# Kernel optimization log

Measured on AMD Instinct MI355X. Metric: run time of the kernel, lower is better.

The kernel has to match this reference:

```python
import jax, jax.numpy as jnp
import numpy as np

N = 100000      # nodes
E = 640000      # edges
V_IN = 128
U_IN = 64
HID = 128
B = 128         # graphs


def setup_inputs() -> dict:
    key = jax.random.key(0)
    ks = jax.random.split(key, 9)
    x = jax.random.normal(ks[0], (N, V_IN), dtype=jnp.float32)
    edge_index = jax.random.randint(ks[1], (2, E), 0, N, dtype=jnp.int64)
    edge_attr = jax.random.normal(ks[2], (E, HID), dtype=jnp.float32)
    u = jax.random.normal(ks[3], (B, U_IN), dtype=jnp.float32)
    batch = jnp.sort(jax.random.randint(ks[4], (N,), 0, B, dtype=jnp.int64))
    fan_in1 = V_IN + HID + U_IN
    W1 = jax.random.normal(ks[5], (fan_in1, HID), dtype=jnp.float32) / np.sqrt(fan_in1)
    b1 = jnp.zeros((HID,), dtype=jnp.float32)
    W2 = jax.random.normal(ks[6], (HID, HID), dtype=jnp.float32) / np.sqrt(HID)
    b2 = jnp.zeros((HID,), dtype=jnp.float32)
    return {"x": x, "edge_index": edge_index, "edge_attr": edge_attr, "u": u,
            "batch": batch, "W1": W1, "b1": b1, "W2": W2, "b2": b2}


def reference(x, edge_index, edge_attr, u, batch, W1, b1, W2, b2):
    col = edge_index[1]
    # scatter_add edge_attr into destination-node slots: [N, HID]
    agg = jax.ops.segment_sum(edge_attr, col, num_segments=x.shape[0])
    # concat [x, agg, u[batch]] -> [N, V_IN + HID + U_IN]
    h = jnp.concatenate([x, agg, u[batch]], axis=1)
    h = jax.nn.relu(h @ W1 + b1)
    return h @ W2 + b2
```

## Files before the change

kernel.cpp:

```cpp
#include <hip/hip_runtime.h>
#include <hip/hip_bf16.h>

#define V_IN 128
#define U_IN 64
#define HID 128
#define K1  (V_IN + HID + U_IN)

typedef __attribute__((ext_vector_type(8))) short bf16x8;
typedef __attribute__((ext_vector_type(4))) float f32x4;

static __device__ __forceinline__ unsigned short f2bf(float f) {
    __hip_bfloat16 h = __float2bfloat16(f);
    union { __hip_bfloat16 h; unsigned short u; } v; v.h = h;
    return v.u;
}
static __device__ __forceinline__ unsigned int f2bf2(float lo, float hi) {
    __hip_bfloat162 h2 = __float22bfloat162_rn(make_float2(lo, hi));
    union { __hip_bfloat162 h; unsigned int u; } v; v.h = h2;
    return v.u;
}

__global__ __launch_bounds__(256) void zero_prep(
    const float* __restrict__ W1, const float* __restrict__ W2,
    unsigned short* __restrict__ Wt1, unsigned short* __restrict__ Wt2,
    int* __restrict__ deg, int N)
{
    int id = blockIdx.x * 256 + threadIdx.x;
    if (id < N) deg[id] = 0;
    if (id < HID * K1) {
        int c = id / K1, k = id - c * K1;
        Wt1[id] = f2bf(W1[(size_t)k * HID + c]);
    }
    if (id < HID * HID) {
        int c = id >> 7, k = id & 127;
        Wt2[id] = f2bf(W2[(size_t)k * HID + c]);
    }
}


__global__ __launch_bounds__(256) void hist_kernel(
    const int* __restrict__ col, int* __restrict__ deg, int E)
{
    int e = blockIdx.x * 256 + threadIdx.x;
    if (e < E) atomicAdd(&deg[col[e]], 1);
}

__global__ __launch_bounds__(256) void scan_partial(
    const int* __restrict__ deg, int* __restrict__ blockSums, int N)
{
    __shared__ int sdata[256];
    int base = blockIdx.x * 1024;
    int tid  = threadIdx.x;
    int s = 0;
    #pragma unroll
    for (int j = 0; j < 4; ++j) {
        int i = base + tid * 4 + j;
        if (i < N) s += deg[i];
    }
    sdata[tid] = s;
    __syncthreads();
    for (int off = 128; off > 0; off >>= 1) {
        if (tid < off) sdata[tid] += sdata[tid + off];
        __syncthreads();
    }
    if (tid == 0) blockSums[blockIdx.x] = sdata[0];
}

__global__ __launch_bounds__(256) void scan_final(
    const int* __restrict__ deg, const int* __restrict__ blockSums,
    int* __restrict__ offsets, int* __restrict__ cur, int N, int E)
{
    __shared__ int sdata[256];
    __shared__ int rdata[256];
    int tid = threadIdx.x;

    int part = 0;
    for (int i = tid; i < (int)blockIdx.x; i += 256) part += blockSums[i];
    rdata[tid] = part;
    __syncthreads();
    for (int off = 128; off > 0; off >>= 1) {
        if (tid < off) rdata[tid] += rdata[tid + off];
        __syncthreads();
    }
    const int blockPrefix = rdata[0];

    int base = blockIdx.x * 1024;
    int loc[4];
    int s = 0;
    #pragma unroll
    for (int j = 0; j < 4; ++j) {
        int i = base + tid * 4 + j;
        loc[j] = (i < N) ? deg[i] : 0;
        s += loc[j];
    }
    int mine = s;
    sdata[tid] = s;
    __syncthreads();
    for (int off = 1; off < 256; off <<= 1) {
        int t = (tid >= off) ? sdata[tid - off] : 0;
        __syncthreads();
        sdata[tid] += t;
        __syncthreads();
    }
    int prefix = blockPrefix + sdata[tid] - mine;
    #pragma unroll
    for (int j = 0; j < 4; ++j) {
        int i = base + tid * 4 + j;
        if (i < N) { offsets[i] = prefix; cur[i] = prefix; prefix += loc[j]; }
    }
    if (blockIdx.x == 0 && tid == 0) offsets[N] = E;
}

__global__ __launch_bounds__(256) void fill_kernel(
    const int* __restrict__ col, int* __restrict__ cur,
    int* __restrict__ eidx, int E)
{
    int e = blockIdx.x * 256 + threadIdx.x;
    if (e < E) {
        int p = atomicAdd(&cur[col[e]], 1);
        eidx[p] = e;
    }
}

#define ROWS 32
#define LDA_E 328
#define LDH_E 136
#define ECAP 1280

__global__ __launch_bounds__(512, 4) void mlp_mfma(
    const float* __restrict__ x,
    const float* __restrict__ edge_attr,
    const int*   __restrict__ offsets,
    const int*   __restrict__ eidx,
    const float* __restrict__ u,
    const int*   __restrict__ batch,
    const unsigned short* __restrict__ Wt1,
    const unsigned short* __restrict__ Wt2,
    const float* __restrict__ b1, const float* __restrict__ b2,
    float* __restrict__ out, int N)
{
    __shared__ __align__(16) unsigned short A[ROWS * LDA_E];
    __shared__ __align__(16) unsigned short H[ROWS * LDH_E];
    __shared__ int Eidx[ECAP];
    __shared__ int Soff[ROWS + 1];
    __shared__ int ticket;
    const int tid  = threadIdx.x;
    const int n0   = blockIdx.x * ROWS;
    const int lane = tid & 63;
    const int wave = tid >> 6;
    const int l15  = lane & 15;
    const int lhi  = lane >> 4;
    const int wcol = wave * 16 + l15;

    const int nEnd   = (n0 + ROWS < N) ? n0 + ROWS : N;
    if (tid <= ROWS) {
        int idx = n0 + tid;
        Soff[tid] = offsets[(idx < nEnd) ? idx : nEnd];
    }
    if (tid == 0) ticket = 0;
    const int s_base = offsets[n0];
    const int s_end  = offsets[nEnd];
    const int cnt    = (s_end - s_base < ECAP) ? s_end - s_base : ECAP;
    for (int i = tid; i < cnt; i += 512) Eidx[i] = eidx[s_base + i];

    #pragma unroll
    for (int it = 0; it < 3; ++it) {
        int t   = tid + it * 512;
        int row = t / 48;
        int s   = t - row * 48;
        int n   = n0 + row;
        unsigned short* Arow = &A[row * LDA_E];
        float4 v = make_float4(0.f, 0.f, 0.f, 0.f);
        int colbase;
        if (s < 32) {
            if (n < N) v = ((const float4*)(x + (size_t)n * V_IN))[s];
            colbase = s * 4;
        } else {
            if (n < N) {
                int b = batch[n];
                v = ((const float4*)(u + (size_t)b * U_IN))[s - 32];
            }
            colbase = V_IN + HID + (s - 32) * 4;
        }
        uint2 o; o.x = f2bf2(v.x, v.y); o.y = f2bf2(v.z, v.w);
        *(uint2*)&Arow[colbase] = o;
    }
    __syncthreads();

    {
        const int c = tid & 31;
        for (;;) {
            int r;
            if (c == 0) r = atomicAdd(&ticket, 1);
            r = __shfl(r, 0, 32);
            if (r >= ROWS) break;
            int n = n0 + r;
            f32x4 a0 = {0.f, 0.f, 0.f, 0.f};
            f32x4 a1 = {0.f, 0.f, 0.f, 0.f};
            f32x4 a2 = {0.f, 0.f, 0.f, 0.f};
            f32x4 a3 = {0.f, 0.f, 0.f, 0.f};
            if (n < N) {
                int ls = Soff[r]     - s_base;
                int le = Soff[r + 1] - s_base;
                int j = ls;
                for (; j + 3 < le; j += 4) {
                    int e0, e1, e2, e3;
                    if (j + 3 < ECAP) {
                        e0 = Eidx[j];     e1 = Eidx[j + 1];
                        e2 = Eidx[j + 2]; e3 = Eidx[j + 3];
                    } else {
                        e0 = eidx[s_base + j];     e1 = eidx[s_base + j + 1];
                        e2 = eidx[s_base + j + 2]; e3 = eidx[s_base + j + 3];
                    }
                    f32x4 v0 = __builtin_nontemporal_load((const f32x4*)(edge_attr + (size_t)e0 * HID) + c);
                    f32x4 v1 = __builtin_nontemporal_load((const f32x4*)(edge_attr + (size_t)e1 * HID) + c);
                    f32x4 v2 = __builtin_nontemporal_load((const f32x4*)(edge_attr + (size_t)e2 * HID) + c);
                    f32x4 v3 = __builtin_nontemporal_load((const f32x4*)(edge_attr + (size_t)e3 * HID) + c);
                    a0 += v0; a1 += v1; a2 += v2; a3 += v3;
                }
                for (; j < le; ++j) {
                    int e0 = (j < ECAP) ? Eidx[j] : eidx[s_base + j];
                    a0 += __builtin_nontemporal_load((const f32x4*)(edge_attr + (size_t)e0 * HID) + c);
                }
            }
            f32x4 asum = (a0 + a1) + (a2 + a3);
            uint2 o;
            o.x = f2bf2(asum[0], asum[1]);
            o.y = f2bf2(asum[2], asum[3]);
            *(uint2*)&A[r * LDA_E + V_IN + c * 4] = o;
        }
    }

    bf16x8 w1f[10], w2f[4];
    #pragma unroll
    for (int ks = 0; ks < 10; ++ks)
        w1f[ks] = *(const bf16x8*)(Wt1 + (size_t)wcol * K1 + ks * 32 + lhi * 8);
    #pragma unroll
    for (int ks = 0; ks < 4; ++ks)
        w2f[ks] = *(const bf16x8*)(Wt2 + (size_t)wcol * HID + ks * 32 + lhi * 8);
    const float b1v = b1[wcol];
    const float b2v = b2[wcol];

    __syncthreads();

    f32x4 acc[2] = {{0.f, 0.f, 0.f, 0.f}, {0.f, 0.f, 0.f, 0.f}};
    #pragma unroll
    for (int ks = 0; ks < 10; ++ks) {
        #pragma unroll
        for (int h = 0; h < 2; ++h) {
            bf16x8 af = *(const bf16x8*)&A[(h * 16 + l15) * LDA_E + ks * 32 + lhi * 8];
            acc[h] = __builtin_amdgcn_mfma_f32_16x16x32_bf16(af, w1f[ks], acc[h], 0, 0, 0);
        }
    }
    #pragma unroll
    for (int h = 0; h < 2; ++h)
        #pragma unroll
        for (int r = 0; r < 4; ++r) {
            float hv = fmaxf(acc[h][r] + b1v, 0.f);
            H[(h * 16 + lhi * 4 + r) * LDH_E + wcol] = f2bf(hv);
        }
    __syncthreads();

    f32x4 acc2[2] = {{0.f, 0.f, 0.f, 0.f}, {0.f, 0.f, 0.f, 0.f}};
    #pragma unroll
    for (int ks = 0; ks < 4; ++ks) {
        #pragma unroll
        for (int h = 0; h < 2; ++h) {
            bf16x8 hf = *(const bf16x8*)&H[(h * 16 + l15) * LDH_E + ks * 32 + lhi * 8];
            acc2[h] = __builtin_amdgcn_mfma_f32_16x16x32_bf16(hf, w2f[ks], acc2[h], 0, 0, 0);
        }
    }
    #pragma unroll
    for (int h = 0; h < 2; ++h)
        #pragma unroll
        for (int r = 0; r < 4; ++r) {
            int n = n0 + h * 16 + lhi * 4 + r;
            if (n < N) out[(size_t)n * HID + wcol] = acc2[h][r] + b2v;
        }
}

extern "C" void kernel_launch(void* const* d_in, const int* in_sizes, int n_in,
                              void* d_out, int out_size, void* d_ws, size_t ws_size,
                              hipStream_t stream) {
    const float* x          = (const float*)d_in[0];
    const int*   edge_index = (const int*)  d_in[1];
    const float* edge_attr  = (const float*)d_in[2];
    const float* u          = (const float*)d_in[3];
    const int*   batch      = (const int*)  d_in[4];
    const float* W1         = (const float*)d_in[5];
    const float* b1         = (const float*)d_in[6];
    const float* W2         = (const float*)d_in[7];
    const float* b2         = (const float*)d_in[8];
    float* out = (float*)d_out;

    const int N = in_sizes[0] / V_IN;
    const int E = in_sizes[1] / 2;
    const int* col = edge_index + E;

    unsigned short* Wt1  = (unsigned short*)d_ws;
    unsigned short* Wt2  = Wt1 + (size_t)K1 * HID;
    int* deg       = (int*)(Wt2 + (size_t)HID * HID);
    int* cur       = deg + N;
    int* offsets   = cur + N;
    int* blockSums = offsets + N + 1;
    int* eidx      = blockSums + 2048;

    const int NB = (N + 1023) / 1024;
    const int ZP = ((N > HID * K1 ? N : HID * K1) + 255) / 256;

    zero_prep   <<<ZP, 256, 0, stream>>>(W1, W2, Wt1, Wt2, deg, N);
    hist_kernel <<<(E + 255) / 256, 256, 0, stream>>>(col, deg, E);
    scan_partial<<<NB, 256, 0, stream>>>(deg, blockSums, N);
    scan_final  <<<NB, 256, 0, stream>>>(deg, blockSums, offsets, cur, N, E);
    fill_kernel <<<(E + 255) / 256, 256, 0, stream>>>(col, cur, eidx, E);

    mlp_mfma<<<(N + ROWS - 1) / ROWS, 512, 0, stream>>>(
        x, edge_attr, offsets, eidx, u, batch, Wt1, Wt2, b1, b2, out, N);
}
```

Baseline: 203.6 us.

## Fuse CSR build stages into one cooperative kernel with grid syncs

The five separate preprocessing launches (zero/weight prep, degree histogram, two-pass scan, fill) are merged into a single cooperative kernel of 1024 blocks that separates the phases with grid-wide syncs and uses grid-stride loops. This removes the per-launch overhead and gaps between kernels, at the cost of grid barrier latency and a fixed grid size that must be co-resident. Separately, the edge_attr gathers in the MLP kernel drop the nontemporal hint and use plain loads, which changes cache behaviour for the gathered rows.

New measurement: 598.7 us. +194.1%, slower.

```diff
diff --git a/kernel.cpp b/kernel.cpp
--- a/kernel.cpp
+++ b/kernel.cpp
@@ -1,5 +1,8 @@
 #include <hip/hip_runtime.h>
 #include <hip/hip_bf16.h>
+#include <hip/hip_cooperative_groups.h>
+
+namespace cg = cooperative_groups;
 
 #define V_IN 128
 #define U_IN 64
@@ -20,103 +23,93 @@
     return v.u;
 }
 
-__global__ __launch_bounds__(256) void zero_prep(
+__global__ __launch_bounds__(256) void csr_build(
     const float* __restrict__ W1, const float* __restrict__ W2,
     unsigned short* __restrict__ Wt1, unsigned short* __restrict__ Wt2,
-    int* __restrict__ deg, int N)
+    int* __restrict__ deg, int* __restrict__ cur,
+    int* __restrict__ offsets, int* __restrict__ blockSums,
+    int* __restrict__ eidx, const int* __restrict__ col,
+    int N, int E, int NB)
 {
-    int id = blockIdx.x * 256 + threadIdx.x;
-    if (id < N) deg[id] = 0;
-    if (id < HID * K1) {
-        int c = id / K1, k = id - c * K1;
-        Wt1[id] = f2bf(W1[(size_t)k * HID + c]);
-    }
-    if (id < HID * HID) {
-        int c = id >> 7, k = id & 127;
-        Wt2[id] = f2bf(W2[(size_t)k * HID + c]);
-    }
-}
-
-
-__global__ __launch_bounds__(256) void hist_kernel(
-    const int* __restrict__ col, int* __restrict__ deg, int E)
-{
-    int e = blockIdx.x * 256 + threadIdx.x;
-    if (e < E) atomicAdd(&deg[col[e]], 1);
-}
-
-__global__ __launch_bounds__(256) void scan_partial(
-    const int* __restrict__ deg, int* __restrict__ blockSums, int N)
-{
-    __shared__ int sdata[256];
-    int base = blockIdx.x * 1024;
-    int tid  = threadIdx.x;
-    int s = 0;
-    #pragma unroll
-    for (int j = 0; j < 4; ++j) {
-        int i = base + tid * 4 + j;
-        if (i < N) s += deg[i];
-    }
-    sdata[tid] = s;
-    __syncthreads();
-    for (int off = 128; off > 0; off >>= 1) {
-        if (tid < off) sdata[tid] += sdata[tid + off];
-        __syncthreads();
-    }
-    if (tid == 0) blockSums[blockIdx.x] = sdata[0];
-}
-
-__global__ __launch_bounds__(256) void scan_final(
-    const int* __restrict__ deg, const int* __restrict__ blockSums,
-    int* __restrict__ offsets, int* __restrict__ cur, int N, int E)
-{
+    cg::grid_group grid = cg::this_grid();
     __shared__ int sdata[256];
     __shared__ int rdata[256];
-    int tid = threadIdx.x;
-
-    int part = 0;
-    for (int i = tid; i < (int)blockIdx.x; i += 256) part += blockSums[i];
-    rdata[tid] = part;
-    __syncthreads();
-    for (int off = 128; off > 0; off >>= 1) {
-        if (tid < off) rdata[tid] += rdata[tid + off];
+    const int tid = threadIdx.x;
+    const int gid = blockIdx.x * 256 + tid;
+    const int gsz = gridDim.x * 256;
+
+    for (int i = gid; i < N; i += gsz) deg[i] = 0;
+    for (int i = gid; i < HID * K1; i += gsz) {
+        int c = i / K1, k = i - c * K1;
+        Wt1[i] = f2bf(W1[(size_t)k * HID + c]);
+    }
+    for (int i = gid; i < HID * HID; i += gsz) {
+        int c = i >> 7, k = i & 127;
+        Wt2[i] = f2bf(W2[(size_t)k * HID + c]);
+    }
+    grid.sync();
+
+    for (int e = gid; e < E; e += gsz) atomicAdd(&deg[col[e]], 1);
+    grid.sync();
+
+    if ((int)blockIdx.x < NB) {
+        int base = blockIdx.x * 1024;
+        int s = 0;
+        #pragma unroll
+        for (int j = 0; j < 4; ++j) {
+            int i = base + tid * 4 + j;
+            if (i < N) s += deg[i];
+        }
+        sdata[tid] = s;
         __syncthreads();
-    }
-    const int blockPrefix = rdata[0];
-
-    int base = blockIdx.x * 1024;
-    int loc[4];
-    int s = 0;
-    #pragma unroll
-    for (int j = 0; j < 4; ++j) {
-        int i = base + tid * 4 + j;
-        loc[j] = (i < N) ? deg[i] : 0;
-        s += loc[j];
-    }
-    int mine = s;
-    sdata[tid] = s;
-    __syncthreads();
-    for (int off = 1; off < 256; off <<= 1) {
-        int t = (tid >= off) ? sdata[tid - off] : 0;
+        for (int off = 128; off > 0; off >>= 1) {
+            if (tid < off) sdata[tid] += sdata[tid + off];
+            __syncthreads();
+        }
+        if (tid == 0) blockSums[blockIdx.x] = sdata[0];
+    }
+    grid.sync();
+
+    if ((int)blockIdx.x < NB) {
+        int part = 0;
+        for (int i = tid; i < (int)blockIdx.x; i += 256) part += blockSums[i];
+        rdata[tid] = part;
         __syncthreads();
-        sdata[tid] += t;
+        for (int off = 128; off > 0; off >>= 1) {
+            if (tid < off) rdata[tid] += rdata[tid + off];
+            __syncthreads();
+        }
+        const int blockPrefix = rdata[0];
+
+        int base = blockIdx.x * 1024;
+        int loc[4];
+        int s = 0;
+        #pragma unroll
+        for (int j = 0; j < 4; ++j) {
+            int i = base + tid * 4 + j;
+            loc[j] = (i < N) ? deg[i] : 0;
+            s += loc[j];
+        }
+        int mine = s;
+        sdata[tid] = s;
         __syncthreads();
-    }
-    int prefix = blockPrefix + sdata[tid] - mine;
-    #pragma unroll
-    for (int j = 0; j < 4; ++j) {
-        int i = base + tid * 4 + j;
-        if (i < N) { offsets[i] = prefix; cur[i] = prefix; prefix += loc[j]; }
-    }
-    if (blockIdx.x == 0 && tid == 0) offsets[N] = E;
-}
-
-__global__ __launch_bounds__(256) void fill_kernel(
-    const int* __restrict__ col, int* __restrict__ cur,
-    int* __restrict__ eidx, int E)
-{
-    int e = blockIdx.x * 256 + threadIdx.x;
-    if (e < E) {
+        for (int off = 1; off < 256; off <<= 1) {
+            int t = (tid >= off) ? sdata[tid - off] : 0;
+            __syncthreads();
+            sdata[tid] += t;
+            __syncthreads();
+        }
+        int prefix = blockPrefix + sdata[tid] - mine;
+        #pragma unroll
+        for (int j = 0; j < 4; ++j) {
+            int i = base + tid * 4 + j;
+            if (i < N) { offsets[i] = prefix; cur[i] = prefix; prefix += loc[j]; }
+        }
+    }
+    if (gid == 0) offsets[N] = E;
+    grid.sync();
+
+    for (int e = gid; e < E; e += gsz) {
         int p = atomicAdd(&cur[col[e]], 1);
         eidx[p] = e;
     }
@@ -212,15 +205,15 @@
                         e0 = eidx[s_base + j];     e1 = eidx[s_base + j + 1];
                         e2 = eidx[s_base + j + 2]; e3 = eidx[s_base + j + 3];
                     }
-                    f32x4 v0 = __builtin_nontemporal_load((const f32x4*)(edge_attr + (size_t)e0 * HID) + c);
-                    f32x4 v1 = __builtin_nontemporal_load((const f32x4*)(edge_attr + (size_t)e1 * HID) + c);
-                    f32x4 v2 = __builtin_nontemporal_load((const f32x4*)(edge_attr + (size_t)e2 * HID) + c);
-                    f32x4 v3 = __builtin_nontemporal_load((const f32x4*)(edge_attr + (size_t)e3 * HID) + c);
+                    f32x4 v0 = *((const f32x4*)(edge_attr + (size_t)e0 * HID) + c);
+                    f32x4 v1 = *((const f32x4*)(edge_attr + (size_t)e1 * HID) + c);
+                    f32x4 v2 = *((const f32x4*)(edge_attr + (size_t)e2 * HID) + c);
+                    f32x4 v3 = *((const f32x4*)(edge_attr + (size_t)e3 * HID) + c);
                     a0 += v0; a1 += v1; a2 += v2; a3 += v3;
                 }
                 for (; j < le; ++j) {
                     int e0 = (j < ECAP) ? Eidx[j] : eidx[s_base + j];
-                    a0 += __builtin_nontemporal_load((const f32x4*)(edge_attr + (size_t)e0 * HID) + c);
+                    a0 += *((const f32x4*)(edge_attr + (size_t)e0 * HID) + c);
                 }
             }
             f32x4 asum = (a0 + a1) + (a2 + a3);
@@ -305,14 +298,16 @@
     int* blockSums = offsets + N + 1;
     int* eidx      = blockSums + 2048;
 
-    const int NB = (N + 1023) / 1024;
-    const int ZP = ((N > HID * K1 ? N : HID * K1) + 255) / 256;
-
-    zero_prep   <<<ZP, 256, 0, stream>>>(W1, W2, Wt1, Wt2, deg, N);
-    hist_kernel <<<(E + 255) / 256, 256, 0, stream>>>(col, deg, E);
-    scan_partial<<<NB, 256, 0, stream>>>(deg, blockSums, N);
-    scan_final  <<<NB, 256, 0, stream>>>(deg, blockSums, offsets, cur, N, E);
-    fill_kernel <<<(E + 255) / 256, 256, 0, stream>>>(col, cur, eidx, E);
+    int NB = (N + 1023) / 1024;
+    int Nv = N, Ev = E;
+
+    void* args[] = {
+        (void*)&W1, (void*)&W2, (void*)&Wt1, (void*)&Wt2,
+        (void*)&deg, (void*)&cur, (void*)&offsets, (void*)&blockSums,
+        (void*)&eidx, (void*)&col, (void*)&Nv, (void*)&Ev, (void*)&NB
+    };
+    hipLaunchCooperativeKernel((const void*)csr_build,
+                               dim3(1024), dim3(256), args, 0, stream);
 
     mlp_mfma<<<(N + ROWS - 1) / ROWS, 512, 0, stream>>>(
         x, edge_attr, offsets, eidx, u, batch, Wt1, Wt2, b1, b2, out, N);
```
